# Optimization experiments

Measured on AMD Instinct MI355X. Metric: run time of the kernel, lower is better.

Reference implementation:

```python
import jax, jax.numpy as jnp
import numpy as np

N_NODES = 100000
N_EDGES = 1600000
IN_CH = 128
HID = 128   # 2 * out_channels
OUT = 64


def setup_inputs() -> dict:
    key = jax.random.key(0)
    ks = jax.random.split(key, 5)
    x = jax.random.normal(ks[0], (N_NODES, IN_CH), dtype=jnp.float32)
    edge_index = jax.random.randint(ks[1], (2, N_EDGES), 0, N_NODES, dtype=jnp.int64)
    # Glorot-ish init for the two GCN weight matrices
    W1 = jax.random.normal(ks[2], (IN_CH, HID), dtype=jnp.float32) / np.sqrt(IN_CH)
    b1 = jnp.zeros((HID,), dtype=jnp.float32)
    W2 = jax.random.normal(ks[3], (HID, OUT), dtype=jnp.float32) / np.sqrt(HID)
    b2 = jnp.zeros((OUT,), dtype=jnp.float32)
    return {"x": x, "edge_index": edge_index, "W1": W1, "b1": b1, "W2": W2, "b2": b2}


def _gcn_conv(x, W, b, src, dst, coef, n):
    # Standard GCNConv: D^{-1/2} (A + I) D^{-1/2} X W + b
    xw = x @ W                                   # [N, F_out]
    msg = xw[src] * coef[:, None]                # gather + scale  [E+N, F_out]
    agg = jax.ops.segment_sum(msg, dst, num_segments=n)  # scatter-add [N, F_out]
    return agg + b


def reference(x, edge_index, W1, b1, W2, b2):
    n = x.shape[0]
    loops = jnp.arange(n, dtype=edge_index.dtype)
    src = jnp.concatenate([edge_index[0], loops])  # add self loops
    dst = jnp.concatenate([edge_index[1], loops])
    deg = jax.ops.segment_sum(jnp.ones_like(src, dtype=x.dtype), dst, num_segments=n)
    dinv = jnp.where(deg > 0, jax.lax.rsqrt(deg), 0.0)
    coef = dinv[src] * dinv[dst]                  # symmetric normalization per edge

    h = _gcn_conv(x, W1, b1, src, dst, coef, n)
    h = jax.nn.relu(h)                            # non_linearity=True
    # F.normalize(p=2, dim=-1) with eps clamp 1e-12; dropout inactive (eval mode)
    h = h / jnp.maximum(jnp.linalg.norm(h, axis=-1, keepdims=True), 1e-12)
    return _gcn_conv(h, W2, b2, src, dst, coef, n)
```

## Files before the change

kernel.cpp:

```cpp
#include <hip/hip_runtime.h>
#include <hip/hip_bf16.h>


#define IN_CH 128
#define HID 128
#define OUT_CH 64
#define NBLK 128
#define MAXNB 1568

typedef unsigned int uint_t;
typedef unsigned short ushort_t;
typedef __attribute__((ext_vector_type(8))) short bf16x8;
typedef __attribute__((ext_vector_type(4))) float f32x4;

__device__ __forceinline__ ushort_t f32_to_bf16_rn(float f) {
    uint_t u = __float_as_uint(f);
    u = (u + 0x7fffu + ((u >> 16) & 1u)) >> 16;
    return (ushort_t)u;
}
__device__ __forceinline__ float bf16lo_to_f32(uint_t u) { return __uint_as_float(u << 16); }
__device__ __forceinline__ float bf16hi_to_f32(uint_t u) { return __uint_as_float(u & 0xffff0000u); }

__global__ __launch_bounds__(256) void hist_kernel(const int* __restrict__ dst, int E,
                                                   int chunk, int NB,
                                                   int* __restrict__ blk_cnt) {
    __shared__ int hist[MAXNB];
    int tid = threadIdx.x;
    int blk = blockIdx.x;
    for (int b = tid; b < NB; b += 256) hist[b] = 0;
    __syncthreads();
    int start = blk * chunk;
    int end = start + chunk; if (end > E) end = E;
    int e = start + tid;
    for (; e + 768 < end; e += 1024) {
        int d0 = dst[e], d1 = dst[e + 256], d2 = dst[e + 512], d3 = dst[e + 768];
        atomicAdd(&hist[d0 >> 6], 1);
        atomicAdd(&hist[d1 >> 6], 1);
        atomicAdd(&hist[d2 >> 6], 1);
        atomicAdd(&hist[d3 >> 6], 1);
    }
    for (; e < end; e += 256) atomicAdd(&hist[dst[e] >> 6], 1);
    __syncthreads();
    for (int b = tid; b < NB; b += 256) blk_cnt[blk * NB + b] = hist[b];
}

__global__ __launch_bounds__(256) void btot_kernel(const int* __restrict__ blk_cnt,
                                                   int NB, int* __restrict__ btot) {
    int b = blockIdx.x * 256 + threadIdx.x;
    if (b < NB) {
        int sum = 0;
        #pragma unroll 8
        for (int blk = 0; blk < NBLK; blk++) sum += blk_cnt[blk * NB + b];
        btot[b] = sum;
    }
}

__global__ __launch_bounds__(256) void scan_kernel(const int* __restrict__ btot, int NB,
                                                   int* __restrict__ bucket_base,
                                                   int* __restrict__ row_start,
                                                   int n, int E) {
    __shared__ int sdata[256];
    __shared__ int carryS;
    int tid = threadIdx.x;
    if (tid == 0) carryS = 0;
    __syncthreads();
    int nchunks = (NB + 255) / 256;
    for (int c = 0; c < nchunks; c++) {
        int i = c * 256 + tid;
        int v = (i < NB) ? btot[i] : 0;
        sdata[tid] = v;
        __syncthreads();
        for (int off = 1; off < 256; off <<= 1) {
            int t = (tid >= off) ? sdata[tid - off] : 0;
            __syncthreads();
            sdata[tid] += t;
            __syncthreads();
        }
        if (i < NB) bucket_base[i] = carryS + sdata[tid] - v;
        __syncthreads();
        if (tid == 0) carryS += sdata[255];
        __syncthreads();
    }
    if (tid == 0) {
        bucket_base[NB] = E;
        row_start[n] = E;
    }
}

__global__ __launch_bounds__(256) void colscan_kernel(const int* __restrict__ blk_cnt,
                                                      const int* __restrict__ bucket_base,
                                                      int NB, int* __restrict__ blk_start) {
    __shared__ int tile[NBLK][16];
    int tid = threadIdx.x;
    int b0 = blockIdx.x * 16;
    for (int idx = tid; idx < NBLK * 16; idx += 256) {
        int blk = idx >> 4, b = idx & 15;
        if (b0 + b < NB) tile[blk][b] = blk_cnt[blk * NB + b0 + b];
    }
    __syncthreads();
    if (tid < 16 && b0 + tid < NB) {
        int running = bucket_base[b0 + tid];
        for (int blk = 0; blk < NBLK; blk++) {
            int t = tile[blk][tid];
            tile[blk][tid] = running;
            running += t;
        }
    }
    __syncthreads();
    for (int idx = tid; idx < NBLK * 16; idx += 256) {
        int blk = idx >> 4, b = idx & 15;
        if (b0 + b < NB) blk_start[blk * NB + b0 + b] = tile[blk][b];
    }
}

__global__ __launch_bounds__(256) void scatter_kernel(const int* __restrict__ src,
                                                      const int* __restrict__ dst,
                                                      int E, int chunk, int NB,
                                                      const int* __restrict__ blk_start,
                                                      uint_t* __restrict__ pairs) {
    __shared__ int cur[MAXNB];
    int tid = threadIdx.x;
    int blk = blockIdx.x;
    for (int b = tid; b < NB; b += 256) cur[b] = blk_start[blk * NB + b];
    __syncthreads();
    int start = blk * chunk;
    int end = start + chunk; if (end > E) end = E;
    int e = start + tid;
    for (; e + 768 < end; e += 1024) {
        int d0 = dst[e], d1 = dst[e + 256], d2 = dst[e + 512], d3 = dst[e + 768];
        int s0 = src[e], s1 = src[e + 256], s2 = src[e + 512], s3 = src[e + 768];
        int p0 = atomicAdd(&cur[d0 >> 6], 1);
        int p1 = atomicAdd(&cur[d1 >> 6], 1);
        int p2 = atomicAdd(&cur[d2 >> 6], 1);
        int p3 = atomicAdd(&cur[d3 >> 6], 1);
        pairs[p0] = (uint_t)s0 | ((uint_t)(d0 & 63) << 26);
        pairs[p1] = (uint_t)s1 | ((uint_t)(d1 & 63) << 26);
        pairs[p2] = (uint_t)s2 | ((uint_t)(d2 & 63) << 26);
        pairs[p3] = (uint_t)s3 | ((uint_t)(d3 & 63) << 26);
    }
    for (; e < end; e += 256) {
        int d = dst[e], s = src[e];
        int p = atomicAdd(&cur[d >> 6], 1);
        pairs[p] = (uint_t)s | ((uint_t)(d & 63) << 26);
    }
}

__global__ __launch_bounds__(256) void fine_fill_kernel(const uint_t* __restrict__ pairs,
                                                        const int* __restrict__ bucket_base,
                                                        int* __restrict__ row_start,
                                                        float* __restrict__ dinv,
                                                        int* __restrict__ csr_src,
                                                        int n) {
    __shared__ int cnt64[64];
    __shared__ int cur[64];
    int b = blockIdx.x;
    int node0 = b << 6;
    int tid = threadIdx.x;
    if (tid < 64) cnt64[tid] = 0;
    __syncthreads();
    int start = bucket_base[b];
    int end = bucket_base[b + 1];
    int e = start + tid;
    for (; e + 768 < end; e += 1024) {
        uint_t u0 = pairs[e], u1 = pairs[e + 256], u2 = pairs[e + 512], u3 = pairs[e + 768];
        atomicAdd(&cnt64[u0 >> 26], 1);
        atomicAdd(&cnt64[u1 >> 26], 1);
        atomicAdd(&cnt64[u2 >> 26], 1);
        atomicAdd(&cnt64[u3 >> 26], 1);
    }
    for (; e < end; e += 256) atomicAdd(&cnt64[pairs[e] >> 26], 1);
    __syncthreads();
    if (tid < 64) {
        int c = cnt64[tid];
        int v = c;
        #pragma unroll
        for (int off = 1; off < 64; off <<= 1) {
            int u = __shfl_up(v, off, 64);
            if (tid >= off) v += u;
        }
        int excl = start + v - c;
        if (node0 + tid < n) {
            row_start[node0 + tid] = excl;
            dinv[node0 + tid] = rsqrtf((float)(c + 1));
        }
        cur[tid] = excl;
    }
    __syncthreads();
    e = start + tid;
    for (; e + 768 < end; e += 1024) {
        uint_t u0 = pairs[e], u1 = pairs[e + 256], u2 = pairs[e + 512], u3 = pairs[e + 768];
        int p0 = atomicAdd(&cur[u0 >> 26], 1);
        int p1 = atomicAdd(&cur[u1 >> 26], 1);
        int p2 = atomicAdd(&cur[u2 >> 26], 1);
        int p3 = atomicAdd(&cur[u3 >> 26], 1);
        csr_src[p0] = (int)(u0 & 0x3FFFFFFu);
        csr_src[p1] = (int)(u1 & 0x3FFFFFFu);
        csr_src[p2] = (int)(u2 & 0x3FFFFFFu);
        csr_src[p3] = (int)(u3 & 0x3FFFFFFu);
    }
    for (; e < end; e += 256) {
        uint_t u = pairs[e];
        int p = atomicAdd(&cur[u >> 26], 1);
        csr_src[p] = (int)(u & 0x3FFFFFFu);
    }
}

__global__ __launch_bounds__(256) void wsplit_kernel(const float* __restrict__ W1,
                                                     const float* __restrict__ W2,
                                                     ushort_t* __restrict__ w1h,
                                                     ushort_t* __restrict__ w1l,
                                                     ushort_t* __restrict__ w2h,
                                                     ushort_t* __restrict__ w2l) {
    int idx = blockIdx.x * 256 + threadIdx.x;
    const int tot1 = 128 * 128;
    const int tot = tot1 + 64 * 128;
    if (idx >= tot) return;
    float v;
    ushort_t* ph;
    ushort_t* pl;
    int o;
    if (idx < tot1) {
        int c = idx >> 7, k = idx & 127;
        v = W1[k * 128 + c];
        ph = w1h; pl = w1l; o = idx;
    } else {
        int j = idx - tot1;
        int c = j >> 7, k = j & 127;
        v = W2[k * 64 + c];
        ph = w2h; pl = w2l; o = j;
    }
    ushort_t h = f32_to_bf16_rn(v);
    float hv = __uint_as_float((uint_t)h << 16);
    ph[o] = h;
    pl[o] = f32_to_bf16_rn(v - hv);
}

template <int NCOL, bool F32_IN>
__global__ __launch_bounds__(256, 2) void mfma_gemm_kernel(const void* __restrict__ Xv,
                                                           const ushort_t* __restrict__ Wth,
                                                           const ushort_t* __restrict__ Wtl,
                                                           const float* __restrict__ rowscale,
                                                           ushort_t* __restrict__ Y, int n) {
    constexpr int NT = NCOL / 16;
    constexpr int WB = NCOL * 128 * 2;
    constexpr int NCH = WB / 16;
    __shared__ __align__(16) char Bs[2 * WB];

    int tid = threadIdx.x;

    for (int i = tid; i < 2 * NCH; i += 256) {
        bool lo = (i >= NCH);
        int j = lo ? i - NCH : i;
        int row = j >> 4, c = j & 15;
        bf16x8 v = *(const bf16x8*)((lo ? Wtl : Wth) + row * 128 + c * 8);
        int bo = (row << 8) + (c << 4);
        bo ^= (row & 7) << 4;
        *(bf16x8*)(Bs + (lo ? WB : 0) + bo) = v;
    }
    __syncthreads();

    int wave = tid >> 6;
    int lane = tid & 63;
    int q = lane >> 4;
    int r16 = lane & 15;
    int rowBase = blockIdx.x * 128 + wave * 32;
    int ar0 = rowBase + r16;      if (ar0 > n - 1) ar0 = n - 1;
    int ar1 = rowBase + 16 + r16; if (ar1 > n - 1) ar1 = n - 1;

    const float* X = (const float*)Xv;
    const ushort_t* Hb = (const ushort_t*)Xv;

    f32x4 acc[2][NT];
    #pragma unroll
    for (int rt = 0; rt < 2; rt++)
        #pragma unroll
        for (int t = 0; t < NT; t++) acc[rt][t] = (f32x4){0.f, 0.f, 0.f, 0.f};

    #pragma unroll
    for (int ks = 0; ks < 4; ks++) {
        int k0 = ks * 32 + q * 8;
        bf16x8 ah[2], al[2] = {};
        #pragma unroll
        for (int rt = 0; rt < 2; rt++) {
            int arow = rt ? ar1 : ar0;
            if (F32_IN) {
                const float4* xr = (const float4*)(X + (size_t)arow * 128 + k0);
                float4 p0 = xr[0], p1 = xr[1];
                float v[8] = {p0.x, p0.y, p0.z, p0.w, p1.x, p1.y, p1.z, p1.w};
                #pragma unroll
                for (int j = 0; j < 8; j++) {
                    ushort_t hb = f32_to_bf16_rn(v[j]);
                    float hv = __uint_as_float((uint_t)hb << 16);
                    ah[rt][j] = (short)hb;
                    al[rt][j] = (short)f32_to_bf16_rn(v[j] - hv);
                }
            } else {
                ah[rt] = *(const bf16x8*)(Hb + (size_t)arow * 128 + k0);
            }
        }
        #pragma unroll
        for (int t = 0; t < NT; t++) {
            int bo = ((t * 16 + r16) << 8) + ks * 64 + (q << 4);
            bo ^= (r16 & 7) << 4;
            bf16x8 bh = *(const bf16x8*)(Bs + bo);
            bf16x8 bl = *(const bf16x8*)(Bs + WB + bo);
            #pragma unroll
            for (int rt = 0; rt < 2; rt++) {
                acc[rt][t] = __builtin_amdgcn_mfma_f32_16x16x32_bf16(ah[rt], bh, acc[rt][t], 0, 0, 0);
                acc[rt][t] = __builtin_amdgcn_mfma_f32_16x16x32_bf16(ah[rt], bl, acc[rt][t], 0, 0, 0);
                if (F32_IN)
                    acc[rt][t] = __builtin_amdgcn_mfma_f32_16x16x32_bf16(al[rt], bh, acc[rt][t], 0, 0, 0);
            }
        }
    }

    #pragma unroll
    for (int rt = 0; rt < 2; rt++) {
        #pragma unroll
        for (int rr = 0; rr < 4; rr++) {
            int row = rowBase + rt * 16 + q * 4 + rr;
            if (row < n) {
                float rs = rowscale[row];
                #pragma unroll
                for (int t = 0; t < NT; t++)
                    Y[(size_t)row * NCOL + t * 16 + r16] = f32_to_bf16_rn(acc[rt][t][rr] * rs);
            }
        }
    }
}

__global__ __launch_bounds__(256) void agg1_kernel(const ushort_t* __restrict__ xw,
                                                   const int* __restrict__ csr_src,
                                                   const int* __restrict__ row_start,
                                                   const float* __restrict__ dinv,
                                                   const float* __restrict__ b1,
                                                   ushort_t* __restrict__ h, int n) {
    int wid = (blockIdx.x * 256 + threadIdx.x) >> 6;
    int lane = threadIdx.x & 63;
    if (wid >= n) return;
    int i = wid;
    float di = dinv[i];
    int e0 = row_start[i], e1 = row_start[i + 1];
    uint_t su = ((const uint_t*)(xw + (size_t)i * HID))[lane];
    float ax = bf16lo_to_f32(su), ay = bf16hi_to_f32(su);
    int e = e0;
    for (; e + 8 <= e1; e += 8) {
        int s[8];
        #pragma unroll
        for (int j = 0; j < 8; j++) s[j] = csr_src[e + j];
        uint_t v[8];
        #pragma unroll
        for (int j = 0; j < 8; j++)
            v[j] = ((const uint_t*)(xw + (size_t)s[j] * HID))[lane];
        #pragma unroll
        for (int j = 0; j < 8; j++) {
            ax += bf16lo_to_f32(v[j]);
            ay += bf16hi_to_f32(v[j]);
        }
    }
    if (e < e1) {
        int last = e1 - 1;
        int s[8];
        #pragma unroll
        for (int j = 0; j < 8; j++) {
            int idx = e + j;
            s[j] = csr_src[idx <= last ? idx : last];
        }
        uint_t v[8];
        #pragma unroll
        for (int j = 0; j < 8; j++)
            v[j] = ((const uint_t*)(xw + (size_t)s[j] * HID))[lane];
        #pragma unroll
        for (int j = 0; j < 8; j++) {
            float c = (e + j <= last) ? 1.0f : 0.0f;
            ax = fmaf(bf16lo_to_f32(v[j]), c, ax);
            ay = fmaf(bf16hi_to_f32(v[j]), c, ay);
        }
    }
    ax = fmaf(ax, di, b1[lane * 2]);
    ay = fmaf(ay, di, b1[lane * 2 + 1]);
    ax = fmaxf(ax, 0.f);
    ay = fmaxf(ay, 0.f);
    float ss = ax * ax + ay * ay;
    #pragma unroll
    for (int m = 32; m >= 1; m >>= 1) ss += __shfl_xor(ss, m, 64);
    float scale = 1.0f / fmaxf(sqrtf(ss), 1e-12f);
    uint_t u = (uint_t)f32_to_bf16_rn(ax * scale) |
               ((uint_t)f32_to_bf16_rn(ay * scale) << 16);
    ((uint_t*)(h + (size_t)i * HID))[lane] = u;
}

__global__ __launch_bounds__(256) void agg2_kernel(const ushort_t* __restrict__ hw,
                                                   const int* __restrict__ csr_src,
                                                   const int* __restrict__ row_start,
                                                   const float* __restrict__ dinv,
                                                   const float* __restrict__ b2,
                                                   float* __restrict__ out, int n) {
    int wid = (blockIdx.x * 256 + threadIdx.x) >> 6;
    int lane = threadIdx.x & 63;
    int i = wid * 2 + (lane >> 5);
    int l = lane & 31;
    if (i >= n) return;
    float di = dinv[i];
    uint_t su = ((const uint_t*)(hw + (size_t)i * OUT_CH))[l];
    float ax = bf16lo_to_f32(su), ay = bf16hi_to_f32(su);
    int e0 = row_start[i], e1 = row_start[i + 1];
    int e = e0;
    for (; e + 8 <= e1; e += 8) {
        int s[8];
        #pragma unroll
        for (int j = 0; j < 8; j++) s[j] = csr_src[e + j];
        uint_t v[8];
        #pragma unroll
        for (int j = 0; j < 8; j++)
            v[j] = ((const uint_t*)(hw + (size_t)s[j] * OUT_CH))[l];
        #pragma unroll
        for (int j = 0; j < 8; j++) {
            ax += bf16lo_to_f32(v[j]);
            ay += bf16hi_to_f32(v[j]);
        }
    }
    if (e < e1) {
        int last = e1 - 1;
        int s[8];
        #pragma unroll
        for (int j = 0; j < 8; j++) {
            int idx = e + j;
            s[j] = csr_src[idx <= last ? idx : last];
        }
        uint_t v[8];
        #pragma unroll
        for (int j = 0; j < 8; j++)
            v[j] = ((const uint_t*)(hw + (size_t)s[j] * OUT_CH))[l];
        #pragma unroll
        for (int j = 0; j < 8; j++) {
            float c = (e + j <= last) ? 1.0f : 0.0f;
            ax = fmaf(bf16lo_to_f32(v[j]), c, ax);
            ay = fmaf(bf16hi_to_f32(v[j]), c, ay);
        }
    }
    ax = fmaf(ax, di, b2[l * 2]);
    ay = fmaf(ay, di, b2[l * 2 + 1]);
    ((float2*)(out + (size_t)i * OUT_CH))[l] = make_float2(ax, ay);
}

extern "C" void kernel_launch(void* const* d_in, const int* in_sizes, int n_in,
                              void* d_out, int out_size, void* d_ws, size_t ws_size,
                              hipStream_t stream) {
    const float* x  = (const float*)d_in[0];
    const int*   ei = (const int*)d_in[1];
    const float* W1 = (const float*)d_in[2];
    const float* b1 = (const float*)d_in[3];
    const float* W2 = (const float*)d_in[4];
    const float* b2 = (const float*)d_in[5];
    float* out = (float*)d_out;

    const int N = in_sizes[0] / IN_CH;
    const int E = in_sizes[1] / 2;
    const int* src = ei;
    const int* dst = ei + E;
    const int NB = (N + 63) / 64;
    const int chunk = (E + NBLK - 1) / NBLK;

    char* base = (char*)d_ws;
    size_t off = 0;
    auto alloc = [&](size_t bytes) -> void* {
        void* p = base + off;
        off = (off + bytes + 255) & ~(size_t)255;
        return p;
    };
    int*      blk_cnt     = (int*)alloc((size_t)NBLK * NB * 4);
    int*      blk_start   = (int*)alloc((size_t)NBLK * NB * 4);
    int*      btot        = (int*)alloc((size_t)NB * 4);
    int*      bucket_base = (int*)alloc((size_t)(NB + 1) * 4);
    int*      row_start   = (int*)alloc((size_t)(N + 1) * 4);
    float*    dinv        = (float*)alloc((size_t)N * 4);
    int*      csr_src     = (int*)alloc((size_t)E * 4);
    uint_t*   pairs       = (uint_t*)alloc((size_t)E * 4);
    ushort_t* xw          = (ushort_t*)alloc((size_t)N * HID * 2);
    ushort_t* h           = (ushort_t*)alloc((size_t)N * HID * 2);
    ushort_t* hw          = (ushort_t*)alloc((size_t)N * OUT_CH * 2);
    ushort_t* w1h         = (ushort_t*)alloc((size_t)128 * 128 * 2);
    ushort_t* w1l         = (ushort_t*)alloc((size_t)128 * 128 * 2);
    ushort_t* w2h         = (ushort_t*)alloc((size_t)64 * 128 * 2);
    ushort_t* w2l         = (ushort_t*)alloc((size_t)64 * 128 * 2);
    (void)ws_size;

    wsplit_kernel<<<(128 * 128 + 64 * 128 + 255) / 256, 256, 0, stream>>>(
        W1, W2, w1h, w1l, w2h, w2l);

    hist_kernel<<<NBLK, 256, 0, stream>>>(dst, E, chunk, NB, blk_cnt);
    btot_kernel<<<(NB + 255) / 256, 256, 0, stream>>>(blk_cnt, NB, btot);
    scan_kernel<<<1, 256, 0, stream>>>(btot, NB, bucket_base, row_start, N, E);
    colscan_kernel<<<(NB + 15) / 16, 256, 0, stream>>>(blk_cnt, bucket_base, NB, blk_start);
    scatter_kernel<<<NBLK, 256, 0, stream>>>(src, dst, E, chunk, NB, blk_start, pairs);
    fine_fill_kernel<<<NB, 256, 0, stream>>>(pairs, bucket_base, row_start, dinv,
                                             csr_src, N);

    mfma_gemm_kernel<128, true><<<(N + 127) / 128, 256, 0, stream>>>(
        x, w1h, w1l, dinv, xw, N);
    agg1_kernel<<<(N * 64 + 255) / 256, 256, 0, stream>>>(xw, csr_src, row_start,
                                                          dinv, b1, h, N);
    mfma_gemm_kernel<64, false><<<(N + 127) / 128, 256, 0, stream>>>(
        h, w2h, w2l, dinv, hw, N);
    int waves2 = (N + 1) / 2;
    agg2_kernel<<<(waves2 * 64 + 255) / 256, 256, 0, stream>>>(hw, csr_src, row_start,
                                                               dinv, b2, out, N);
}
```

Baseline: 291.7 us.

## Gather rows with 16-byte loads and split edges across lane groups in aggregation

After: 299.3 us. 1.03x slower.

```diff
diff --git a/kernel.cpp b/kernel.cpp
--- a/kernel.cpp
+++ b/kernel.cpp
@@ -12,6 +12,7 @@
 typedef unsigned short ushort_t;
 typedef __attribute__((ext_vector_type(8))) short bf16x8;
 typedef __attribute__((ext_vector_type(4))) float f32x4;
+typedef __attribute__((ext_vector_type(2))) float f32v2;
 
 __device__ __forceinline__ ushort_t f32_to_bf16_rn(float f) {
     uint_t u = __float_as_uint(f);
@@ -339,55 +340,90 @@
     int lane = threadIdx.x & 63;
     if (wid >= n) return;
     int i = wid;
+    int g = lane >> 4;
+    int cb = lane & 15;
+    const uint4* X4 = (const uint4*)xw;
     float di = dinv[i];
     int e0 = row_start[i], e1 = row_start[i + 1];
-    uint_t su = ((const uint_t*)(xw + (size_t)i * HID))[lane];
-    float ax = bf16lo_to_f32(su), ay = bf16hi_to_f32(su);
+
+    f32v2 a0 = {0.f, 0.f}, a1 = {0.f, 0.f}, a2 = {0.f, 0.f}, a3 = {0.f, 0.f};
+    {
+        uint4 v = X4[(size_t)i * 16 + cb];
+        float sc = (g == 0) ? 1.0f : 0.0f;
+        f32v2 scv = {sc, sc};
+        a0 += (f32v2){bf16lo_to_f32(v.x), bf16hi_to_f32(v.x)} * scv;
+        a1 += (f32v2){bf16lo_to_f32(v.y), bf16hi_to_f32(v.y)} * scv;
+        a2 += (f32v2){bf16lo_to_f32(v.z), bf16hi_to_f32(v.z)} * scv;
+        a3 += (f32v2){bf16lo_to_f32(v.w), bf16hi_to_f32(v.w)} * scv;
+    }
     int e = e0;
     for (; e + 8 <= e1; e += 8) {
-        int s[8];
-        #pragma unroll
-        for (int j = 0; j < 8; j++) s[j] = csr_src[e + j];
-        uint_t v[8];
-        #pragma unroll
-        for (int j = 0; j < 8; j++)
-            v[j] = ((const uint_t*)(xw + (size_t)s[j] * HID))[lane];
-        #pragma unroll
-        for (int j = 0; j < 8; j++) {
-            ax += bf16lo_to_f32(v[j]);
-            ay += bf16hi_to_f32(v[j]);
-        }
+        int sa = csr_src[e + g];
+        int sb = csr_src[e + 4 + g];
+        uint4 va = X4[(size_t)sa * 16 + cb];
+        uint4 vb = X4[(size_t)sb * 16 + cb];
+        a0 += (f32v2){bf16lo_to_f32(va.x), bf16hi_to_f32(va.x)};
+        a1 += (f32v2){bf16lo_to_f32(va.y), bf16hi_to_f32(va.y)};
+        a2 += (f32v2){bf16lo_to_f32(va.z), bf16hi_to_f32(va.z)};
+        a3 += (f32v2){bf16lo_to_f32(va.w), bf16hi_to_f32(va.w)};
+        a0 += (f32v2){bf16lo_to_f32(vb.x), bf16hi_to_f32(vb.x)};
+        a1 += (f32v2){bf16lo_to_f32(vb.y), bf16hi_to_f32(vb.y)};
+        a2 += (f32v2){bf16lo_to_f32(vb.z), bf16hi_to_f32(vb.z)};
+        a3 += (f32v2){bf16lo_to_f32(vb.w), bf16hi_to_f32(vb.w)};
+    }
+    if (e + 4 <= e1) {
+        int s = csr_src[e + g];
+        uint4 v = X4[(size_t)s * 16 + cb];
+        a0 += (f32v2){bf16lo_to_f32(v.x), bf16hi_to_f32(v.x)};
+        a1 += (f32v2){bf16lo_to_f32(v.y), bf16hi_to_f32(v.y)};
+        a2 += (f32v2){bf16lo_to_f32(v.z), bf16hi_to_f32(v.z)};
+        a3 += (f32v2){bf16lo_to_f32(v.w), bf16hi_to_f32(v.w)};
+        e += 4;
     }
     if (e < e1) {
         int last = e1 - 1;
-        int s[8];
-        #pragma unroll
-        for (int j = 0; j < 8; j++) {
-            int idx = e + j;
-            s[j] = csr_src[idx <= last ? idx : last];
-        }
-        uint_t v[8];
-        #pragma unroll
-        for (int j = 0; j < 8; j++)
-            v[j] = ((const uint_t*)(xw + (size_t)s[j] * HID))[lane];
-        #pragma unroll
-        for (int j = 0; j < 8; j++) {
-            float c = (e + j <= last) ? 1.0f : 0.0f;
-            ax = fmaf(bf16lo_to_f32(v[j]), c, ax);
-            ay = fmaf(bf16hi_to_f32(v[j]), c, ay);
-        }
-    }
-    ax = fmaf(ax, di, b1[lane * 2]);
-    ay = fmaf(ay, di, b1[lane * 2 + 1]);
-    ax = fmaxf(ax, 0.f);
-    ay = fmaxf(ay, 0.f);
-    float ss = ax * ax + ay * ay;
-    #pragma unroll
-    for (int m = 32; m >= 1; m >>= 1) ss += __shfl_xor(ss, m, 64);
+        int idx = e + g;
+        int s = csr_src[idx <= last ? idx : last];
+        uint4 v = X4[(size_t)s * 16 + cb];
+        float cc = (idx <= last) ? 1.0f : 0.0f;
+        f32v2 cv = {cc, cc};
+        a0 += (f32v2){bf16lo_to_f32(v.x), bf16hi_to_f32(v.x)} * cv;
+        a1 += (f32v2){bf16lo_to_f32(v.y), bf16hi_to_f32(v.y)} * cv;
+        a2 += (f32v2){bf16lo_to_f32(v.z), bf16hi_to_f32(v.z)} * cv;
+        a3 += (f32v2){bf16lo_to_f32(v.w), bf16hi_to_f32(v.w)} * cv;
+    }
+    #pragma unroll
+    for (int m = 16; m <= 32; m <<= 1) {
+        a0.x += __shfl_xor(a0.x, m, 64); a0.y += __shfl_xor(a0.y, m, 64);
+        a1.x += __shfl_xor(a1.x, m, 64); a1.y += __shfl_xor(a1.y, m, 64);
+        a2.x += __shfl_xor(a2.x, m, 64); a2.y += __shfl_xor(a2.y, m, 64);
+        a3.x += __shfl_xor(a3.x, m, 64); a3.y += __shfl_xor(a3.y, m, 64);
+    }
+    const float2* bp = (const float2*)(b1 + cb * 8);
+    float2 b0v = bp[0], b1v = bp[1], b2v = bp[2], b3v = bp[3];
+    float vals[8];
+    vals[0] = fmaxf(fmaf(a0.x, di, b0v.x), 0.f);
+    vals[1] = fmaxf(fmaf(a0.y, di, b0v.y), 0.f);
+    vals[2] = fmaxf(fmaf(a1.x, di, b1v.x), 0.f);
+    vals[3] = fmaxf(fmaf(a1.y, di, b1v.y), 0.f);
+    vals[4] = fmaxf(fmaf(a2.x, di, b2v.x), 0.f);
+    vals[5] = fmaxf(fmaf(a2.y, di, b2v.y), 0.f);
+    vals[6] = fmaxf(fmaf(a3.x, di, b3v.x), 0.f);
+    vals[7] = fmaxf(fmaf(a3.y, di, b3v.y), 0.f);
+    float ss = 0.f;
+    #pragma unroll
+    for (int j = 0; j < 8; j++) ss = fmaf(vals[j], vals[j], ss);
+    #pragma unroll
+    for (int m = 1; m <= 8; m <<= 1) ss += __shfl_xor(ss, m, 64);
     float scale = 1.0f / fmaxf(sqrtf(ss), 1e-12f);
-    uint_t u = (uint_t)f32_to_bf16_rn(ax * scale) |
-               ((uint_t)f32_to_bf16_rn(ay * scale) << 16);
-    ((uint_t*)(h + (size_t)i * HID))[lane] = u;
+    if (g == 0) {
+        uint4 o;
+        o.x = (uint_t)f32_to_bf16_rn(vals[0] * scale) | ((uint_t)f32_to_bf16_rn(vals[1] * scale) << 16);
+        o.y = (uint_t)f32_to_bf16_rn(vals[2] * scale) | ((uint_t)f32_to_bf16_rn(vals[3] * scale) << 16);
+        o.z = (uint_t)f32_to_bf16_rn(vals[4] * scale) | ((uint_t)f32_to_bf16_rn(vals[5] * scale) << 16);
+        o.w = (uint_t)f32_to_bf16_rn(vals[6] * scale) | ((uint_t)f32_to_bf16_rn(vals[7] * scale) << 16);
+        ((uint4*)h)[(size_t)i * 16 + cb] = o;
+    }
 }
 
 __global__ __launch_bounds__(256) void agg2_kernel(const ushort_t* __restrict__ hw,
@@ -398,50 +434,82 @@
                                                    float* __restrict__ out, int n) {
     int wid = (blockIdx.x * 256 + threadIdx.x) >> 6;
     int lane = threadIdx.x & 63;
-    int i = wid * 2 + (lane >> 5);
-    int l = lane & 31;
-    if (i >= n) return;
+    if (wid >= n) return;
+    int i = wid;
+    int g = lane >> 3;
+    int cb = lane & 7;
+    const uint4* H4 = (const uint4*)hw;
     float di = dinv[i];
-    uint_t su = ((const uint_t*)(hw + (size_t)i * OUT_CH))[l];
-    float ax = bf16lo_to_f32(su), ay = bf16hi_to_f32(su);
     int e0 = row_start[i], e1 = row_start[i + 1];
+
+    f32v2 a0 = {0.f, 0.f}, a1 = {0.f, 0.f}, a2 = {0.f, 0.f}, a3 = {0.f, 0.f};
+    {
+        uint4 v = H4[(size_t)i * 8 + cb];
+        float sc = (g == 0) ? 1.0f : 0.0f;
+        f32v2 scv = {sc, sc};
+        a0 += (f32v2){bf16lo_to_f32(v.x), bf16hi_to_f32(v.x)} * scv;
+        a1 += (f32v2){bf16lo_to_f32(v.y), bf16hi_to_f32(v.y)} * scv;
+        a2 += (f32v2){bf16lo_to_f32(v.z), bf16hi_to_f32(v.z)} * scv;
+        a3 += (f32v2){bf16lo_to_f32(v.w), bf16hi_to_f32(v.w)} * scv;
+    }
     int e = e0;
-    for (; e + 8 <= e1; e += 8) {
-        int s[8];
-        #pragma unroll
-        for (int j = 0; j < 8; j++) s[j] = csr_src[e + j];
-        uint_t v[8];
-        #pragma unroll
-        for (int j = 0; j < 8; j++)
-            v[j] = ((const uint_t*)(hw + (size_t)s[j] * OUT_CH))[l];
-        #pragma unroll
-        for (int j = 0; j < 8; j++) {
-            ax += bf16lo_to_f32(v[j]);
-            ay += bf16hi_to_f32(v[j]);
-        }
+    for (; e + 16 <= e1; e += 16) {
+        int sa = csr_src[e + g];
+        int sb = csr_src[e + 8 + g];
+        uint4 va = H4[(size_t)sa * 8 + cb];
+        uint4 vb = H4[(size_t)sb * 8 + cb];
+        a0 += (f32v2){bf16lo_to_f32(va.x), bf16hi_to_f32(va.x)};
+        a1 += (f32v2){bf16lo_to_f32(va.y), bf16hi_to_f32(va.y)};
+        a2 += (f32v2){bf16lo_to_f32(va.z), bf16hi_to_f32(va.z)};
+        a3 += (f32v2){bf16lo_to_f32(va.w), bf16hi_to_f32(va.w)};
+        a0 += (f32v2){bf16lo_to_f32(vb.x), bf16hi_to_f32(vb.x)};
+        a1 += (f32v2){bf16lo_to_f32(vb.y), bf16hi_to_f32(vb.y)};
+        a2 += (f32v2){bf16lo_to_f32(vb.z), bf16hi_to_f32(vb.z)};
+        a3 += (f32v2){bf16lo_to_f32(vb.w), bf16hi_to_f32(vb.w)};
+    }
+    if (e + 8 <= e1) {
+        int s = csr_src[e + g];
+        uint4 v = H4[(size_t)s * 8 + cb];
+        a0 += (f32v2){bf16lo_to_f32(v.x), bf16hi_to_f32(v.x)};
+        a1 += (f32v2){bf16lo_to_f32(v.y), bf16hi_to_f32(v.y)};
+        a2 += (f32v2){bf16lo_to_f32(v.z), bf16hi_to_f32(v.z)};
+        a3 += (f32v2){bf16lo_to_f32(v.w), bf16hi_to_f32(v.w)};
+        e += 8;
     }
     if (e < e1) {
         int last = e1 - 1;
-        int s[8];
-        #pragma unroll
-        for (int j = 0; j < 8; j++) {
-            int idx = e + j;
-            s[j] = csr_src[idx <= last ? idx : last];
-        }
-        uint_t v[8];
-        #pragma unroll
-        for (int j = 0; j < 8; j++)
-            v[j] = ((const uint_t*)(hw + (size_t)s[j] * OUT_CH))[l];
-        #pragma unroll
-        for (int j = 0; j < 8; j++) {
-            float c = (e + j <= last) ? 1.0f : 0.0f;
-            ax = fmaf(bf16lo_to_f32(v[j]), c, ax);
-            ay = fmaf(bf16hi_to_f32(v[j]), c, ay);
-        }
-    }
-    ax = fmaf(ax, di, b2[l * 2]);
-    ay = fmaf(ay, di, b2[l * 2 + 1]);
-    ((float2*)(out + (size_t)i * OUT_CH))[l] = make_float2(ax, ay);
+        int idx = e + g;
+        int s = csr_src[idx <= last ? idx : last];
+        uint4 v = H4[(size_t)s * 8 + cb];
+        float cc = (idx <= last) ? 1.0f : 0.0f;
+        f32v2 cv = {cc, cc};
+        a0 += (f32v2){bf16lo_to_f32(v.x), bf16hi_to_f32(v.x)} * cv;
+        a1 += (f32v2){bf16lo_to_f32(v.y), bf16hi_to_f32(v.y)} * cv;
+        a2 += (f32v2){bf16lo_to_f32(v.z), bf16hi_to_f32(v.z)} * cv;
+        a3 += (f32v2){bf16lo_to_f32(v.w), bf16hi_to_f32(v.w)} * cv;
+    }
+    #pragma unroll
+    for (int m = 8; m <= 32; m <<= 1) {
+        a0.x += __shfl_xor(a0.x, m, 64); a0.y += __shfl_xor(a0.y, m, 64);
+        a1.x += __shfl_xor(a1.x, m, 64); a1.y += __shfl_xor(a1.y, m, 64);
+        a2.x += __shfl_xor(a2.x, m, 64); a2.y += __shfl_xor(a2.y, m, 64);
+        a3.x += __shfl_xor(a3.x, m, 64); a3.y += __shfl_xor(a3.y, m, 64);
+    }
+    if (g == 0) {
+        const float2* bp = (const float2*)(b2 + cb * 8);
+        float2 b0v = bp[0], b1v = bp[1], b2v = bp[2], b3v = bp[3];
+        float4 o0, o1;
+        o0.x = fmaf(a0.x, di, b0v.x);
+        o0.y = fmaf(a0.y, di, b0v.y);
+        o0.z = fmaf(a1.x, di, b1v.x);
+        o0.w = fmaf(a1.y, di, b1v.y);
+        o1.x = fmaf(a2.x, di, b2v.x);
+        o1.y = fmaf(a2.y, di, b2v.y);
+        o1.z = fmaf(a3.x, di, b3v.x);
+        o1.w = fmaf(a3.y, di, b3v.y);
+        ((float4*)out)[(size_t)i * 16 + cb * 2]     = o0;
+        ((float4*)out)[(size_t)i * 16 + cb * 2 + 1] = o1;
+    }
 }
 
 extern "C" void kernel_launch(void* const* d_in, const int* in_sizes, int n_in,
@@ -503,7 +571,6 @@
                                                           dinv, b1, h, N);
     mfma_gemm_kernel<64, false><<<(N + 127) / 128, 256, 0, stream>>>(
         h, w2h, w2l, dinv, hw, N);
-    int waves2 = (N + 1) / 2;
-    agg2_kernel<<<(waves2 * 64 + 255) / 256, 256, 0, stream>>>(hw, csr_src, row_start,
-                                                               dinv, b2, out, N);
-}
+    agg2_kernel<<<(N * 64 + 255) / 256, 256, 0, stream>>>(hw, csr_src, row_start,
+                                                          dinv, b2, out, N);
+}
```
